# Kernel tuning notes

Measured on AMD Instinct MI355X. Metric: run time of the kernel, lower is better.

## Reference

```python
import jax, jax.numpy as jnp
import numpy as np

B, S, D, H, HD, F, V = 16, 512, 256, 8, 32, 682, 32000
EPS = 1.1920928955078125e-07


def rmsnorm(x, w):
    return x * jax.lax.rsqrt(jnp.mean(x * x, axis=-1, keepdims=True) + EPS) * w


def rope(x, cos, sin):
    # interleaved RoPE: even/odd lanes rotated pairwise, re-interleaved
    xe, xo = x[..., ::2], x[..., 1::2]
    return jnp.stack([xe * cos - xo * sin, xe * sin + xo * cos], axis=-1).reshape(x.shape)


def setup_inputs() -> dict:
    key = jax.random.key(0)
    ks = jax.random.split(key, 12)
    def n(k, shape, s=0.02):
        return jax.random.normal(k, shape, jnp.float32) * s
    pos = jnp.arange(S, dtype=jnp.float32)
    inv = 1.0 / (10000.0 ** (jnp.arange(0, HD, 2, dtype=jnp.float32) / HD))
    ang = pos[:, None] * inv[None, :]                      # [S, HD/2]
    cos_tab = jnp.repeat(jnp.cos(ang), 2, axis=-1)         # [S, HD]
    sin_tab = jnp.repeat(jnp.sin(ang), 2, axis=-1)
    mask = jnp.tril(jnp.ones((S, S), jnp.int32))[None, None]  # causal [1,1,S,S]
    return dict(
        emb=n(ks[0], (V, D)),
        pos_emb=n(ks[1], (S, D)),
        attn_norm_w=jnp.ones((D,), jnp.float32),
        wq=n(ks[2], (D, D)), bq=jnp.zeros((D,), jnp.float32),
        wk=n(ks[3], (HD, D)), bk=jnp.zeros((HD,), jnp.float32),
        wv=n(ks[4], (D, D)), bv=jnp.zeros((D,), jnp.float32),
        cos_tab=cos_tab, sin_tab=sin_tab,
        ffn_norm_w=jnp.ones((D,), jnp.float32),
        w_gate=n(ks[5], (F, D)), b_gate=jnp.zeros((F,), jnp.float32),
        w_up=n(ks[6], (F, D)), b_up=jnp.zeros((F,), jnp.float32),
        w_down=n(ks[7], (D, F)), b_down=jnp.zeros((D,), jnp.float32),
        tok_ids=jax.random.randint(ks[8], (B, S), 0, V, jnp.int64),
        mask=mask,
    )


def reference(emb, pos_emb, attn_norm_w, wq, bq, wk, bk, wv, bv, cos_tab, sin_tab,
              ffn_norm_w, w_gate, b_gate, w_up, b_up, w_down, b_down, tok_ids, mask):
    h = emb[tok_ids] + pos_emb                                   # [B,S,D]
    x = rmsnorm(h, attn_norm_w)
    # faithful to trace: direct view [B,S,D] -> [B,H,S,HD] (no transpose)
    q = (x @ wq.T + bq).reshape(B, H, S, HD)
    k = (x @ wk.T + bk)[:, None]                                 # [B,1,S,HD] single KV head
    v = (x @ wv.T + bv).reshape(B, H, S, HD)
    cos = cos_tab[:S, ::2][None, None]                           # [1,1,S,HD/2]
    sin = sin_tab[:S, ::2][None, None]
    qr = rope(q, cos, sin)
    kr = rope(k, cos, sin)[:, 0]                                 # [B,S,HD]
    scores = jnp.einsum('bhsd,btd->bhst', qr, kr) / jnp.sqrt(jnp.float32(HD))
    scores = jnp.where(mask == 0, -jnp.inf, scores)
    attn = jax.nn.softmax(scores, axis=-1)
    o = jnp.einsum('bhst,bhtd->bhsd', attn, v).reshape(B, S, D)
    h2 = o + h
    x2 = rmsnorm(h2, ffn_norm_w)
    g = x2 @ w_gate.T + b_gate
    g = g * jax.nn.sigmoid(g)                                    # SiLU gate
    up = x2 @ w_up.T + b_up
    out = (g * up) @ w_down.T + b_down
    # faithful to trace: residual uses post-norm activation x2, not h2
    return out + x2
```

## Files before the change

### kernel.cpp

```cpp
#include <hip/hip_runtime.h>
#include <hip/hip_bf16.h>
#include <cstddef>
#include <cstdint>

constexpr int Bb = 16, Ss = 512, Dd = 256, Hh = 8, HDd = 32, Ff = 682;
constexpr int FKp = 704;
constexpr float EPSf = 1.1920928955078125e-07f;

typedef short bf8v __attribute__((ext_vector_type(8)));
typedef float f4 __attribute__((ext_vector_type(4)));
using bf16 = __hip_bfloat16;

__device__ inline f4 MFMA(bf8v a, bf8v b, f4 c) {
  return __builtin_amdgcn_mfma_f32_16x16x32_bf16(a, b, c, 0, 0, 0);
}

__global__ __launch_bounds__(256) void k_prep(
    const float* __restrict__ wq, const float* __restrict__ wk,
    const float* __restrict__ wv, const float* __restrict__ wg,
    const float* __restrict__ wu, const float* __restrict__ wd,
    bf16* __restrict__ dqkv, bf16* __restrict__ dgate,
    bf16* __restrict__ dup, bf16* __restrict__ ddown,
    const float* __restrict__ emb, const float* __restrict__ pos,
    const int* __restrict__ tok, const float* __restrict__ w,
    bf16* __restrict__ hb, bf16* __restrict__ xb)
{
  const int b = blockIdx.x, tid = threadIdx.x;
  if (b < 640) {
    const int idx = b * 256 + tid;
    const int row = idx >> 8, col = idx & 255;
    float v;
    if (row < 256)      v = wq[(size_t)row * 256 + col];
    else if (row < 288) v = wk[(size_t)(row - 256) * 256 + col];
    else if (row < 544) v = wv[(size_t)(row - 288) * 256 + col];
    else                v = 0.f;
    dqkv[idx] = __float2bfloat16(v);
  } else if (b < 2176) {
    const bool isg = b < 1408;
    const int idx = (b - (isg ? 640 : 1408)) * 256 + tid;
    const int row = idx >> 8, col = idx & 255;
    const float* src = isg ? wg : wu;
    float v = (row < Ff) ? src[(size_t)row * 256 + col] : 0.f;
    (isg ? dgate : dup)[idx] = __float2bfloat16(v);
  } else if (b < 2880) {
    const int idx = (b - 2176) * 256 + tid;
    const int row = idx / FKp, col = idx - row * FKp;
    float v = (col < Ff) ? wd[(size_t)row * Ff + col] : 0.f;
    ddown[idx] = __float2bfloat16(v);
  } else {
    const int row = b - 2880;
    const int s = row & (Ss - 1);
    const int t = tok[row];
    float v = emb[(size_t)t * Dd + tid] + pos[(size_t)s * Dd + tid];
    float ss = v * v;
    #pragma unroll
    for (int off = 32; off > 0; off >>= 1) ss += __shfl_down(ss, off);
    __shared__ float red[4];
    if ((tid & 63) == 0) red[tid >> 6] = ss;
    __syncthreads();
    const float tot = red[0] + red[1] + red[2] + red[3];
    const float r = rsqrtf(tot * (1.0f / Dd) + EPSf);
    const size_t o = (size_t)row * Dd + tid;
    hb[o] = __float2bfloat16(v);
    xb[o] = __float2bfloat16(v * r * w[tid]);
  }
}

__global__ __launch_bounds__(256) void k_add_norm(
    const bf16* __restrict__ a, const bf16* __restrict__ hb,
    const float* __restrict__ w, bf16* __restrict__ x2b)
{
  const int row = blockIdx.x;
  const int tid = threadIdx.x;
  const size_t off = (size_t)row * Dd + tid;
  const float v = __bfloat162float(a[off]) + __bfloat162float(hb[off]);
  float ss = v * v;
  #pragma unroll
  for (int o = 32; o > 0; o >>= 1) ss += __shfl_down(ss, o);
  __shared__ float red[4];
  if ((tid & 63) == 0) red[tid >> 6] = ss;
  __syncthreads();
  const float tot = red[0] + red[1] + red[2] + red[3];
  const float r = rsqrtf(tot * (1.0f / Dd) + EPSf);
  x2b[off] = __float2bfloat16(v * r * w[tid]);
}

__global__ __launch_bounds__(256) void k_qkv(
    const bf16* __restrict__ A, const bf16* __restrict__ W,
    const float* __restrict__ bias0, const float* __restrict__ bias1,
    const float* __restrict__ bias2,
    const float* __restrict__ cost, const float* __restrict__ sint,
    bf16* __restrict__ ob0, bf16* __restrict__ ob1, bf16* __restrict__ vt)
{
  __shared__ bf16 As[128 * 72];
  __shared__ bf16 Bs[64 * 72];
  const int tid = threadIdx.x, lane = tid & 63, wid = tid >> 6;
  const int l15 = lane & 15, lg = lane >> 4;
  const int m0 = blockIdx.x * 128, n0 = blockIdx.y * 64;
  const int wr = (wid >> 1) * 64, wc = (wid & 1) * 32;
  const int srow = tid >> 3, scol = (tid & 7) * 8;

  f4 acc[4][2];
  #pragma unroll
  for (int i = 0; i < 4; i++)
    #pragma unroll
    for (int j = 0; j < 2; j++) acc[i][j] = (f4){0.f, 0.f, 0.f, 0.f};

  bf8v pa[4], pb[2];
  #pragma unroll
  for (int i = 0; i < 4; i++)
    pa[i] = *(const bf8v*)&A[(size_t)(m0 + srow + i * 32) * 256 + scol];
  #pragma unroll
  for (int i = 0; i < 2; i++)
    pb[i] = *(const bf8v*)&W[(size_t)(n0 + srow + i * 32) * 256 + scol];
  #pragma unroll
  for (int i = 0; i < 4; i++) *(bf8v*)&As[(srow + i * 32) * 72 + scol] = pa[i];
  #pragma unroll
  for (int i = 0; i < 2; i++) *(bf8v*)&Bs[(srow + i * 32) * 72 + scol] = pb[i];
  __syncthreads();

  for (int ks = 0; ks < 4; ks++) {
    if (ks < 3) {
      const int kn = (ks + 1) * 64;
      #pragma unroll
      for (int i = 0; i < 4; i++)
        pa[i] = *(const bf8v*)&A[(size_t)(m0 + srow + i * 32) * 256 + kn + scol];
      #pragma unroll
      for (int i = 0; i < 2; i++)
        pb[i] = *(const bf8v*)&W[(size_t)(n0 + srow + i * 32) * 256 + kn + scol];
    }
    #pragma unroll
    for (int kk = 0; kk < 64; kk += 32) {
      bf8v af[4], bw[2];
      #pragma unroll
      for (int mi = 0; mi < 4; mi++)
        af[mi] = *(const bf8v*)&As[(wr + mi * 16 + l15) * 72 + kk + lg * 8];
      #pragma unroll
      for (int ni = 0; ni < 2; ni++)
        bw[ni] = *(const bf8v*)&Bs[(wc + ni * 16 + l15) * 72 + kk + lg * 8];
      #pragma unroll
      for (int mi = 0; mi < 4; mi++)
        #pragma unroll
        for (int ni = 0; ni < 2; ni++)
          acc[mi][ni] = MFMA(af[mi], bw[ni], acc[mi][ni]);
    }
    __syncthreads();
    if (ks < 3) {
      #pragma unroll
      for (int i = 0; i < 4; i++) *(bf8v*)&As[(srow + i * 32) * 72 + scol] = pa[i];
      #pragma unroll
      for (int i = 0; i < 2; i++) *(bf8v*)&Bs[(srow + i * 32) * 72 + scol] = pb[i];
      __syncthreads();
    }
  }

  #pragma unroll
  for (int mi = 0; mi < 4; mi++) {
    #pragma unroll
    for (int ni = 0; ni < 2; ni++) {
      const int nbase = n0 + wc + ni * 16;
      const int n = nbase + l15;
      if (nbase < 288) {
        #pragma unroll
        for (int r = 0; r < 4; r++) {
          const int m = m0 + wr + mi * 16 + lg * 4 + r;
          float vb2 = acc[mi][ni][r] + (nbase < 256 ? bias0[n] : bias1[n - 256]);
          int s, hd;
          if (nbase < 256) { const int flat = ((m & 511) << 8) + n; s = (flat >> 5) & 511; hd = n & 31; }
          else             { s = m & 511; hd = n - 256; }
          const float c = cost[s * 32 + hd], sn = sint[s * 32 + hd];
          const float other = __shfl_xor(vb2, 1);
          const float res = (n & 1) ? (other * sn + vb2 * c) : (vb2 * c - other * sn);
          if (nbase < 256) ob0[(size_t)m * 256 + n] = __float2bfloat16(res);
          else             ob1[(size_t)m * 32 + hd] = __float2bfloat16(res);
        }
      } else if (nbase < 544) {
        const int rel = n - 288;
        const int hd = rel & 31, rq = rel >> 5;
        const int mb = m0 + wr + mi * 16 + lg * 4;
        const int b = mb >> 9;
        const float bv = bias2[rel];
        #pragma unroll
        for (int r = 0; r < 4; r++) {
          const int s = (mb + r) & 511;
          const int hh2 = s >> 6;
          const int s4 = ((s & 63) << 3) + rq;
          vt[((size_t)(b * Hh + hh2) * HDd + hd) * Ss + s4] =
              __float2bfloat16(acc[mi][ni][r] + bv);
        }
      }
    }
  }
}

__global__ __launch_bounds__(256) void k_ffn(
    const bf16* __restrict__ A, const bf16* __restrict__ Wg,
    const bf16* __restrict__ Wu,
    const float* __restrict__ bg, const float* __restrict__ bu,
    bf16* __restrict__ out)
{
  __shared__ bf16 As[128 * 72];
  __shared__ bf16 Gs[64 * 72];
  __shared__ bf16 Us[64 * 72];
  const int tid = threadIdx.x, lane = tid & 63, wid = tid >> 6;
  const int l15 = lane & 15, lg = lane >> 4;
  const int m0 = blockIdx.x * 128, n0 = blockIdx.y * 64;
  const int wr = (wid >> 1) * 64, wc = (wid & 1) * 32;
  const int srow = tid >> 3, scol = (tid & 7) * 8;

  f4 accg[4][2], accu[4][2];
  #pragma unroll
  for (int i = 0; i < 4; i++)
    #pragma unroll
    for (int j = 0; j < 2; j++) {
      accg[i][j] = (f4){0.f, 0.f, 0.f, 0.f};
      accu[i][j] = (f4){0.f, 0.f, 0.f, 0.f};
    }

  bf8v pa[4], pg[2], pu[2];
  #pragma unroll
  for (int i = 0; i < 4; i++)
    pa[i] = *(const bf8v*)&A[(size_t)(m0 + srow + i * 32) * 256 + scol];
  #pragma unroll
  for (int i = 0; i < 2; i++) {
    pg[i] = *(const bf8v*)&Wg[(size_t)(n0 + srow + i * 32) * 256 + scol];
    pu[i] = *(const bf8v*)&Wu[(size_t)(n0 + srow + i * 32) * 256 + scol];
  }
  #pragma unroll
  for (int i = 0; i < 4; i++) *(bf8v*)&As[(srow + i * 32) * 72 + scol] = pa[i];
  #pragma unroll
  for (int i = 0; i < 2; i++) {
    *(bf8v*)&Gs[(srow + i * 32) * 72 + scol] = pg[i];
    *(bf8v*)&Us[(srow + i * 32) * 72 + scol] = pu[i];
  }
  __syncthreads();

  for (int ks = 0; ks < 4; ks++) {
    if (ks < 3) {
      const int kn = (ks + 1) * 64;
      #pragma unroll
      for (int i = 0; i < 4; i++)
        pa[i] = *(const bf8v*)&A[(size_t)(m0 + srow + i * 32) * 256 + kn + scol];
      #pragma unroll
      for (int i = 0; i < 2; i++) {
        pg[i] = *(const bf8v*)&Wg[(size_t)(n0 + srow + i * 32) * 256 + kn + scol];
        pu[i] = *(const bf8v*)&Wu[(size_t)(n0 + srow + i * 32) * 256 + kn + scol];
      }
    }
    #pragma unroll
    for (int kk = 0; kk < 64; kk += 32) {
      bf8v af[4], bgf[2], buf[2];
      #pragma unroll
      for (int mi = 0; mi < 4; mi++)
        af[mi] = *(const bf8v*)&As[(wr + mi * 16 + l15) * 72 + kk + lg * 8];
      #pragma unroll
      for (int ni = 0; ni < 2; ni++) {
        bgf[ni] = *(const bf8v*)&Gs[(wc + ni * 16 + l15) * 72 + kk + lg * 8];
        buf[ni] = *(const bf8v*)&Us[(wc + ni * 16 + l15) * 72 + kk + lg * 8];
      }
      #pragma unroll
      for (int mi = 0; mi < 4; mi++)
        #pragma unroll
        for (int ni = 0; ni < 2; ni++) {
          accg[mi][ni] = MFMA(af[mi], bgf[ni], accg[mi][ni]);
          accu[mi][ni] = MFMA(af[mi], buf[ni], accu[mi][ni]);
        }
    }
    __syncthreads();
    if (ks < 3) {
      #pragma unroll
      for (int i = 0; i < 4; i++) *(bf8v*)&As[(srow + i * 32) * 72 + scol] = pa[i];
      #pragma unroll
      for (int i = 0; i < 2; i++) {
        *(bf8v*)&Gs[(srow + i * 32) * 72 + scol] = pg[i];
        *(bf8v*)&Us[(srow + i * 32) * 72 + scol] = pu[i];
      }
      __syncthreads();
    }
  }

  #pragma unroll
  for (int ni = 0; ni < 2; ni++) {
    const int n = n0 + wc + ni * 16 + l15;
    const float bgv = (n < Ff) ? bg[n] : 0.f;
    const float buv = (n < Ff) ? bu[n] : 0.f;
    #pragma unroll
    for (int mi = 0; mi < 4; mi++) {
      #pragma unroll
      for (int r = 0; r < 4; r++) {
        const int m = m0 + wr + mi * 16 + lg * 4 + r;
        float res = 0.f;
        if (n < Ff) {
          const float gv = accg[mi][ni][r] + bgv;
          const float uv = accu[mi][ni][r] + buv;
          res = gv / (1.f + __expf(-gv)) * uv;
        }
        out[(size_t)m * FKp + n] = __float2bfloat16(res);
      }
    }
  }
}

__global__ __launch_bounds__(256) void k_down(
    const bf16* __restrict__ A, const bf16* __restrict__ W,
    const float* __restrict__ bias, const bf16* __restrict__ resid,
    float* __restrict__ out)
{
  __shared__ bf16 As[64 * 72];
  __shared__ bf16 Bs[64 * 72];
  const int tid = threadIdx.x, lane = tid & 63, wid = tid >> 6;
  const int l15 = lane & 15, lg = lane >> 4;
  const int m0 = blockIdx.x * 64, n0 = blockIdx.y * 64;
  const int wr = (wid >> 1) * 32, wc = (wid & 1) * 32;
  const int srow = tid >> 3, scol = (tid & 7) * 8;

  f4 acc[2][2];
  #pragma unroll
  for (int i = 0; i < 2; i++)
    #pragma unroll
    for (int j = 0; j < 2; j++) acc[i][j] = (f4){0.f, 0.f, 0.f, 0.f};

  bf8v pa[2], pb[2];
  #pragma unroll
  for (int i = 0; i < 2; i++) {
    pa[i] = *(const bf8v*)&A[(size_t)(m0 + srow + i * 32) * FKp + scol];
    pb[i] = *(const bf8v*)&W[(size_t)(n0 + srow + i * 32) * FKp + scol];
  }
  #pragma unroll
  for (int i = 0; i < 2; i++) {
    *(bf8v*)&As[(srow + i * 32) * 72 + scol] = pa[i];
    *(bf8v*)&Bs[(srow + i * 32) * 72 + scol] = pb[i];
  }
  __syncthreads();

  for (int ks = 0; ks < 11; ks++) {
    if (ks < 10) {
      const int kn = (ks + 1) * 64;
      #pragma unroll
      for (int i = 0; i < 2; i++) {
        pa[i] = *(const bf8v*)&A[(size_t)(m0 + srow + i * 32) * FKp + kn + scol];
        pb[i] = *(const bf8v*)&W[(size_t)(n0 + srow + i * 32) * FKp + kn + scol];
      }
    }
    #pragma unroll
    for (int kk = 0; kk < 64; kk += 32) {
      bf8v af[2], bw[2];
      #pragma unroll
      for (int mi = 0; mi < 2; mi++)
        af[mi] = *(const bf8v*)&As[(wr + mi * 16 + l15) * 72 + kk + lg * 8];
      #pragma unroll
      for (int ni = 0; ni < 2; ni++)
        bw[ni] = *(const bf8v*)&Bs[(wc + ni * 16 + l15) * 72 + kk + lg * 8];
      #pragma unroll
      for (int mi = 0; mi < 2; mi++)
        #pragma unroll
        for (int ni = 0; ni < 2; ni++)
          acc[mi][ni] = MFMA(af[mi], bw[ni], acc[mi][ni]);
    }
    __syncthreads();
    if (ks < 10) {
      #pragma unroll
      for (int i = 0; i < 2; i++) {
        *(bf8v*)&As[(srow + i * 32) * 72 + scol] = pa[i];
        *(bf8v*)&Bs[(srow + i * 32) * 72 + scol] = pb[i];
      }
      __syncthreads();
    }
  }

  #pragma unroll
  for (int ni = 0; ni < 2; ni++) {
    const int n = n0 + wc + ni * 16 + l15;
    const float bv = bias[n];
    #pragma unroll
    for (int mi = 0; mi < 2; mi++) {
      #pragma unroll
      for (int r = 0; r < 4; r++) {
        const int m = m0 + wr + mi * 16 + lg * 4 + r;
        out[(size_t)m * 256 + n] = acc[mi][ni][r] + bv +
            __bfloat162float(resid[(size_t)m * 256 + n]);
      }
    }
  }
}

__global__ __launch_bounds__(64) void k_attn_mfma(
    const bf16* __restrict__ q, const bf16* __restrict__ k,
    const bf16* __restrict__ vt, bf16* __restrict__ o)
{
  __shared__ bf16 Ps[16 * 72];
  const int lane = threadIdx.x;
  const int l15 = lane & 15, lg = lane >> 4;
  const int hh = blockIdx.y, bb = blockIdx.z;
  const int bh = bb * Hh + hh;
  const int qrow = (31 - blockIdx.x) * 16;
  const int lt = (qrow + 15) >> 6;
  const float scale = 0.17677669529663687f;

  const bf16* kg = k + (size_t)bb * Ss * HDd;
  const bf16* vg = vt + (size_t)bh * (Ss * HDd);

  const bf8v qf = *(const bf8v*)&q[((size_t)bh * Ss + qrow + l15) * HDd + lg * 8];

  f4 oacc[2];
  oacc[0] = (f4){0.f, 0.f, 0.f, 0.f};
  oacc[1] = (f4){0.f, 0.f, 0.f, 0.f};
  float m = -3.0e38f, l = 0.f;

  for (int ti = 0; ti <= lt; ti++) {
    const int t0 = ti * 64;

    f4 sf[4];
    __builtin_amdgcn_s_setprio(1);
    #pragma unroll
    for (int tf = 0; tf < 4; tf++) {
      const bf8v kf = *(const bf8v*)&kg[(size_t)(t0 + tf * 16 + l15) * HDd + lg * 8];
      sf[tf] = MFMA(kf, qf, (f4){0.f, 0.f, 0.f, 0.f});
    }
    __builtin_amdgcn_s_setprio(0);

    bf8v vb[2][2];
    #pragma unroll
    for (int kt = 0; kt < 2; kt++)
      #pragma unroll
      for (int hf = 0; hf < 2; hf++)
        vb[kt][hf] = *(const bf8v*)&vg[(size_t)(hf * 16 + l15) * Ss + t0 + kt * 32 + lg * 8];

    float pm = -3.0e38f;
    if (ti == lt) {
      #pragma unroll
      for (int tf = 0; tf < 4; tf++)
        #pragma unroll
        for (int r = 0; r < 4; r++) {
          float sv = sf[tf][r] * scale;
          if (t0 + tf * 16 + lg * 4 + r > qrow + l15) sv = -3.0e38f;
          sf[tf][r] = sv;
          pm = fmaxf(pm, sv);
        }
    } else {
      #pragma unroll
      for (int tf = 0; tf < 4; tf++)
        #pragma unroll
        for (int r = 0; r < 4; r++) {
          const float sv = sf[tf][r] * scale;
          sf[tf][r] = sv;
          pm = fmaxf(pm, sv);
        }
    }
    pm = fmaxf(pm, __shfl_xor(pm, 16));
    pm = fmaxf(pm, __shfl_xor(pm, 32));

    const float nm = fmaxf(m, pm);
    const float corr = __expf(m - nm);
    m = nm;

    float ls = 0.f;
    #pragma unroll
    for (int tf = 0; tf < 4; tf++)
      #pragma unroll
      for (int r = 0; r < 4; r++) {
        const float p = __expf(sf[tf][r] - m);
        sf[tf][r] = p;
        ls += p;
      }
    ls += __shfl_xor(ls, 16);
    ls += __shfl_xor(ls, 32);
    l = l * corr + ls;

    #pragma unroll
    for (int tf = 0; tf < 4; tf++) {
      bf16 t4[4];
      #pragma unroll
      for (int r = 0; r < 4; r++) t4[r] = __float2bfloat16(sf[tf][r]);
      *(uint2*)&Ps[l15 * 72 + tf * 16 + lg * 4] = *(const uint2*)t4;
    }

    float corrT[4];
    #pragma unroll
    for (int r = 0; r < 4; r++) corrT[r] = __shfl(corr, lg * 4 + r);
    #pragma unroll
    for (int hf = 0; hf < 2; hf++)
      #pragma unroll
      for (int r = 0; r < 4; r++) oacc[hf][r] *= corrT[r];

    __builtin_amdgcn_s_setprio(1);
    #pragma unroll
    for (int kt = 0; kt < 2; kt++) {
      const bf8v pv = *(const bf8v*)&Ps[l15 * 72 + kt * 32 + lg * 8];
      #pragma unroll
      for (int hf = 0; hf < 2; hf++)
        oacc[hf] = MFMA(pv, vb[kt][hf], oacc[hf]);
    }
    __builtin_amdgcn_s_setprio(0);
  }

  float lT[4];
  #pragma unroll
  for (int r = 0; r < 4; r++) lT[r] = __shfl(l, lg * 4 + r);
  #pragma unroll
  for (int hf = 0; hf < 2; hf++)
    #pragma unroll
    for (int r = 0; r < 4; r++)
      o[((size_t)bh * Ss + qrow + lg * 4 + r) * HDd + hf * 16 + l15] =
          __float2bfloat16(oacc[hf][r] / lT[r]);
}

extern "C" void kernel_launch(void* const* d_in, const int* in_sizes, int n_in,
                              void* d_out, int out_size, void* d_ws, size_t ws_size,
                              hipStream_t stream)
{
  const float* emb     = (const float*)d_in[0];
  const float* pos_emb = (const float*)d_in[1];
  const float* attn_w  = (const float*)d_in[2];
  const float* wq      = (const float*)d_in[3];
  const float* bq      = (const float*)d_in[4];
  const float* wk      = (const float*)d_in[5];
  const float* bk      = (const float*)d_in[6];
  const float* wv      = (const float*)d_in[7];
  const float* bv      = (const float*)d_in[8];
  const float* cos_t   = (const float*)d_in[9];
  const float* sin_t   = (const float*)d_in[10];
  const float* ffn_w   = (const float*)d_in[11];
  const float* w_gate  = (const float*)d_in[12];
  const float* b_gate  = (const float*)d_in[13];
  const float* w_up    = (const float*)d_in[14];
  const float* b_up    = (const float*)d_in[15];
  const float* w_down  = (const float*)d_in[16];
  const float* b_down  = (const float*)d_in[17];
  const int*   tok     = (const int*)d_in[18];
  float* out = (float*)d_out;

  const size_t NT = (size_t)Bb * Ss;
  char* base = (char*)d_ws;
  size_t off = 0;
  auto alloc = [&](size_t bytes) {
    void* r = base + off;
    off = (off + bytes + 255) & ~(size_t)255;
    return r;
  };
  bf16*  h_bf   = (bf16*)alloc(NT * Dd * 2);
  bf16*  x_bf   = (bf16*)alloc(NT * Dd * 2);
  bf16*  q_bf   = (bf16*)alloc(NT * Dd * 2);
  bf16*  k_bf   = (bf16*)alloc(NT * HDd * 2);
  bf16*  vt_bf  = (bf16*)alloc(NT * Dd * 2);
  bf16*  o_bf   = (bf16*)alloc(NT * Dd * 2);
  bf16*  x2_bf  = (bf16*)alloc(NT * Dd * 2);
  bf16*  g_bf   = (bf16*)alloc(NT * (size_t)FKp * 2);
  bf16*  wqkv_b = (bf16*)alloc((size_t)640 * 256 * 2);
  bf16*  wgate_b= (bf16*)alloc((size_t)768 * 256 * 2);
  bf16*  wup_b  = (bf16*)alloc((size_t)768 * 256 * 2);
  bf16*  wdown_b= (bf16*)alloc((size_t)256 * FKp * 2);

  k_prep<<<dim3(2880 + NT), 256, 0, stream>>>(
      wq, wk, wv, w_gate, w_up, w_down, wqkv_b, wgate_b, wup_b, wdown_b,
      emb, pos_emb, tok, attn_w, h_bf, x_bf);

  k_qkv<<<dim3(NT / 128, 10), 256, 0, stream>>>(
      x_bf, wqkv_b, bq, bk, bv, cos_t, sin_t, q_bf, k_bf, vt_bf);

  k_attn_mfma<<<dim3(32, Hh, Bb), 64, 0, stream>>>(q_bf, k_bf, vt_bf, o_bf);

  k_add_norm<<<dim3(NT), 256, 0, stream>>>(o_bf, h_bf, ffn_w, x2_bf);

  k_ffn<<<dim3(NT / 128, 11), 256, 0, stream>>>(
      x2_bf, wgate_b, wup_b, b_gate, b_up, g_bf);

  k_down<<<dim3(NT / 64, 4), 256, 0, stream>>>(
      g_bf, wdown_b, b_down, x2_bf, out);
}
```

Measured before the change: 90.47 us.

## Stage GEMM tiles via direct global-to-LDS loads in qkv, ffn, down kernels

Replaces the register-staged, software-prefetched global->LDS copy in the three GEMM kernels with global_load_lds 16-byte direct loads into unpadded 64-wide LDS rows. This removes the VGPR round trip and LDS store instructions, which may lower register pressure. In exchange it drops the prefetch overlap: each k-step now loads and then waits at a barrier before computing. It also removes the 72-element padding, so the fragment reads may now hit LDS bank conflicts.

```diff
diff --git a/kernel.cpp b/kernel.cpp
--- a/kernel.cpp
+++ b/kernel.cpp
@@ -13,6 +13,12 @@
 
 __device__ inline f4 MFMA(bf8v a, bf8v b, f4 c) {
   return __builtin_amdgcn_mfma_f32_16x16x32_bf16(a, b, c, 0, 0, 0);
+}
+
+__device__ __forceinline__ void gl_lds16(const bf16* g, bf16* l) {
+  __builtin_amdgcn_global_load_lds(
+      (const __attribute__((address_space(1))) unsigned int*)(g),
+      (__attribute__((address_space(3))) unsigned int*)(l), 16, 0, 0);
 }
 
 __global__ __launch_bounds__(256) void k_prep(
@@ -92,13 +98,13 @@
     const float* __restrict__ cost, const float* __restrict__ sint,
     bf16* __restrict__ ob0, bf16* __restrict__ ob1, bf16* __restrict__ vt)
 {
-  __shared__ bf16 As[128 * 72];
-  __shared__ bf16 Bs[64 * 72];
-  const int tid = threadIdx.x, lane = tid & 63, wid = tid >> 6;
+  __shared__ bf16 As[128 * 64];
+  __shared__ bf16 Bs[64 * 64];
+  const int tid = threadIdx.x, lane = tid & 63, wv = tid >> 6;
   const int l15 = lane & 15, lg = lane >> 4;
   const int m0 = blockIdx.x * 128, n0 = blockIdx.y * 64;
-  const int wr = (wid >> 1) * 64, wc = (wid & 1) * 32;
-  const int srow = tid >> 3, scol = (tid & 7) * 8;
+  const int wr = (wv >> 1) * 64, wc = (wv & 1) * 32;
+  const int sr8 = lane >> 3, slot = lane & 7;
 
   f4 acc[4][2];
   #pragma unroll
@@ -106,52 +112,37 @@
     #pragma unroll
     for (int j = 0; j < 2; j++) acc[i][j] = (f4){0.f, 0.f, 0.f, 0.f};
 
-  bf8v pa[4], pb[2];
-  #pragma unroll
-  for (int i = 0; i < 4; i++)
-    pa[i] = *(const bf8v*)&A[(size_t)(m0 + srow + i * 32) * 256 + scol];
-  #pragma unroll
-  for (int i = 0; i < 2; i++)
-    pb[i] = *(const bf8v*)&W[(size_t)(n0 + srow + i * 32) * 256 + scol];
-  #pragma unroll
-  for (int i = 0; i < 4; i++) *(bf8v*)&As[(srow + i * 32) * 72 + scol] = pa[i];
-  #pragma unroll
-  for (int i = 0; i < 2; i++) *(bf8v*)&Bs[(srow + i * 32) * 72 + scol] = pb[i];
-  __syncthreads();
-
   for (int ks = 0; ks < 4; ks++) {
-    if (ks < 3) {
-      const int kn = (ks + 1) * 64;
-      #pragma unroll
-      for (int i = 0; i < 4; i++)
-        pa[i] = *(const bf8v*)&A[(size_t)(m0 + srow + i * 32) * 256 + kn + scol];
-      #pragma unroll
-      for (int i = 0; i < 2; i++)
-        pb[i] = *(const bf8v*)&W[(size_t)(n0 + srow + i * 32) * 256 + kn + scol];
-    }
+    const int k0 = ks * 64;
+    #pragma unroll
+    for (int i = 0; i < 4; i++) {
+      const int row = wv * 32 + i * 8 + sr8;
+      gl_lds16(&A[(size_t)(m0 + row) * 256 + k0 + slot * 8],
+               &As[(wv * 32 + i * 8) * 64]);
+    }
+    #pragma unroll
+    for (int i = 0; i < 2; i++) {
+      const int row = wv * 16 + i * 8 + sr8;
+      gl_lds16(&W[(size_t)(n0 + row) * 256 + k0 + slot * 8],
+               &Bs[(wv * 16 + i * 8) * 64]);
+    }
+    __syncthreads();
     #pragma unroll
     for (int kk = 0; kk < 64; kk += 32) {
       bf8v af[4], bw[2];
       #pragma unroll
       for (int mi = 0; mi < 4; mi++)
-        af[mi] = *(const bf8v*)&As[(wr + mi * 16 + l15) * 72 + kk + lg * 8];
+        af[mi] = *(const bf8v*)&As[(wr + mi * 16 + l15) * 64 + kk + lg * 8];
       #pragma unroll
       for (int ni = 0; ni < 2; ni++)
-        bw[ni] = *(const bf8v*)&Bs[(wc + ni * 16 + l15) * 72 + kk + lg * 8];
+        bw[ni] = *(const bf8v*)&Bs[(wc + ni * 16 + l15) * 64 + kk + lg * 8];
       #pragma unroll
       for (int mi = 0; mi < 4; mi++)
         #pragma unroll
         for (int ni = 0; ni < 2; ni++)
           acc[mi][ni] = MFMA(af[mi], bw[ni], acc[mi][ni]);
     }
-    __syncthreads();
-    if (ks < 3) {
-      #pragma unroll
-      for (int i = 0; i < 4; i++) *(bf8v*)&As[(srow + i * 32) * 72 + scol] = pa[i];
-      #pragma unroll
-      for (int i = 0; i < 2; i++) *(bf8v*)&Bs[(srow + i * 32) * 72 + scol] = pb[i];
-      __syncthreads();
-    }
+    if (ks < 3) __syncthreads();
   }
 
   #pragma unroll
@@ -199,14 +190,14 @@
     const float* __restrict__ bg, const float* __restrict__ bu,
     bf16* __restrict__ out)
 {
-  __shared__ bf16 As[128 * 72];
-  __shared__ bf16 Gs[64 * 72];
-  __shared__ bf16 Us[64 * 72];
-  const int tid = threadIdx.x, lane = tid & 63, wid = tid >> 6;
+  __shared__ bf16 As[128 * 64];
+  __shared__ bf16 Gs[64 * 64];
+  __shared__ bf16 Us[64 * 64];
+  const int tid = threadIdx.x, lane = tid & 63, wv = tid >> 6;
   const int l15 = lane & 15, lg = lane >> 4;
   const int m0 = blockIdx.x * 128, n0 = blockIdx.y * 64;
-  const int wr = (wid >> 1) * 64, wc = (wid & 1) * 32;
-  const int srow = tid >> 3, scol = (tid & 7) * 8;
+  const int wr = (wv >> 1) * 64, wc = (wv & 1) * 32;
+  const int sr8 = lane >> 3, slot = lane & 7;
 
   f4 accg[4][2], accu[4][2];
   #pragma unroll
@@ -217,46 +208,33 @@
       accu[i][j] = (f4){0.f, 0.f, 0.f, 0.f};
     }
 
-  bf8v pa[4], pg[2], pu[2];
-  #pragma unroll
-  for (int i = 0; i < 4; i++)
-    pa[i] = *(const bf8v*)&A[(size_t)(m0 + srow + i * 32) * 256 + scol];
-  #pragma unroll
-  for (int i = 0; i < 2; i++) {
-    pg[i] = *(const bf8v*)&Wg[(size_t)(n0 + srow + i * 32) * 256 + scol];
-    pu[i] = *(const bf8v*)&Wu[(size_t)(n0 + srow + i * 32) * 256 + scol];
-  }
-  #pragma unroll
-  for (int i = 0; i < 4; i++) *(bf8v*)&As[(srow + i * 32) * 72 + scol] = pa[i];
-  #pragma unroll
-  for (int i = 0; i < 2; i++) {
-    *(bf8v*)&Gs[(srow + i * 32) * 72 + scol] = pg[i];
-    *(bf8v*)&Us[(srow + i * 32) * 72 + scol] = pu[i];
-  }
-  __syncthreads();
-
   for (int ks = 0; ks < 4; ks++) {
-    if (ks < 3) {
-      const int kn = (ks + 1) * 64;
-      #pragma unroll
-      for (int i = 0; i < 4; i++)
-        pa[i] = *(const bf8v*)&A[(size_t)(m0 + srow + i * 32) * 256 + kn + scol];
-      #pragma unroll
-      for (int i = 0; i < 2; i++) {
-        pg[i] = *(const bf8v*)&Wg[(size_t)(n0 + srow + i * 32) * 256 + kn + scol];
-        pu[i] = *(const bf8v*)&Wu[(size_t)(n0 + srow + i * 32) * 256 + kn + scol];
-      }
-    }
+    const int k0 = ks * 64;
+    #pragma unroll
+    for (int i = 0; i < 4; i++) {
+      const int row = wv * 32 + i * 8 + sr8;
+      gl_lds16(&A[(size_t)(m0 + row) * 256 + k0 + slot * 8],
+               &As[(wv * 32 + i * 8) * 64]);
+    }
+    #pragma unroll
+    for (int i = 0; i < 2; i++) {
+      const int row = wv * 16 + i * 8 + sr8;
+      gl_lds16(&Wg[(size_t)(n0 + row) * 256 + k0 + slot * 8],
+               &Gs[(wv * 16 + i * 8) * 64]);
+      gl_lds16(&Wu[(size_t)(n0 + row) * 256 + k0 + slot * 8],
+               &Us[(wv * 16 + i * 8) * 64]);
+    }
+    __syncthreads();
     #pragma unroll
     for (int kk = 0; kk < 64; kk += 32) {
       bf8v af[4], bgf[2], buf[2];
       #pragma unroll
       for (int mi = 0; mi < 4; mi++)
-        af[mi] = *(const bf8v*)&As[(wr + mi * 16 + l15) * 72 + kk + lg * 8];
+        af[mi] = *(const bf8v*)&As[(wr + mi * 16 + l15) * 64 + kk + lg * 8];
       #pragma unroll
       for (int ni = 0; ni < 2; ni++) {
-        bgf[ni] = *(const bf8v*)&Gs[(wc + ni * 16 + l15) * 72 + kk + lg * 8];
-        buf[ni] = *(const bf8v*)&Us[(wc + ni * 16 + l15) * 72 + kk + lg * 8];
+        bgf[ni] = *(const bf8v*)&Gs[(wc + ni * 16 + l15) * 64 + kk + lg * 8];
+        buf[ni] = *(const bf8v*)&Us[(wc + ni * 16 + l15) * 64 + kk + lg * 8];
       }
       #pragma unroll
       for (int mi = 0; mi < 4; mi++)
@@ -266,17 +244,7 @@
           accu[mi][ni] = MFMA(af[mi], buf[ni], accu[mi][ni]);
         }
     }
-    __syncthreads();
-    if (ks < 3) {
-      #pragma unroll
-      for (int i = 0; i < 4; i++) *(bf8v*)&As[(srow + i * 32) * 72 + scol] = pa[i];
-      #pragma unroll
-      for (int i = 0; i < 2; i++) {
-        *(bf8v*)&Gs[(srow + i * 32) * 72 + scol] = pg[i];
-        *(bf8v*)&Us[(srow + i * 32) * 72 + scol] = pu[i];
-      }
-      __syncthreads();
-    }
+    if (ks < 3) __syncthreads();
   }
 
   #pragma unroll
@@ -306,13 +274,13 @@
     const float* __restrict__ bias, const bf16* __restrict__ resid,
     float* __restrict__ out)
 {
-  __shared__ bf16 As[64 * 72];
-  __shared__ bf16 Bs[64 * 72];
-  const int tid = threadIdx.x, lane = tid & 63, wid = tid >> 6;
+  __shared__ bf16 As[64 * 64];
+  __shared__ bf16 Bs[64 * 64];
+  const int tid = threadIdx.x, lane = tid & 63, wv = tid >> 6;
   const int l15 = lane & 15, lg = lane >> 4;
   const int m0 = blockIdx.x * 64, n0 = blockIdx.y * 64;
-  const int wr = (wid >> 1) * 32, wc = (wid & 1) * 32;
-  const int srow = tid >> 3, scol = (tid & 7) * 8;
+  const int wr = (wv >> 1) * 32, wc = (wv & 1) * 32;
+  const int sr8 = lane >> 3, slot = lane & 7;
 
   f4 acc[2][2];
   #pragma unroll
@@ -320,52 +288,33 @@
     #pragma unroll
     for (int j = 0; j < 2; j++) acc[i][j] = (f4){0.f, 0.f, 0.f, 0.f};
 
-  bf8v pa[2], pb[2];
-  #pragma unroll
-  for (int i = 0; i < 2; i++) {
-    pa[i] = *(const bf8v*)&A[(size_t)(m0 + srow + i * 32) * FKp + scol];
-    pb[i] = *(const bf8v*)&W[(size_t)(n0 + srow + i * 32) * FKp + scol];
-  }
-  #pragma unroll
-  for (int i = 0; i < 2; i++) {
-    *(bf8v*)&As[(srow + i * 32) * 72 + scol] = pa[i];
-    *(bf8v*)&Bs[(srow + i * 32) * 72 + scol] = pb[i];
-  }
-  __syncthreads();
-
   for (int ks = 0; ks < 11; ks++) {
-    if (ks < 10) {
-      const int kn = (ks + 1) * 64;
-      #pragma unroll
-      for (int i = 0; i < 2; i++) {
-        pa[i] = *(const bf8v*)&A[(size_t)(m0 + srow + i * 32) * FKp + kn + scol];
-        pb[i] = *(const bf8v*)&W[(size_t)(n0 + srow + i * 32) * FKp + kn + scol];
-      }
-    }
+    const int k0 = ks * 64;
+    #pragma unroll
+    for (int i = 0; i < 2; i++) {
+      const int rowa = wv * 16 + i * 8 + sr8;
+      gl_lds16(&A[(size_t)(m0 + rowa) * FKp + k0 + slot * 8],
+               &As[(wv * 16 + i * 8) * 64]);
+      gl_lds16(&W[(size_t)(n0 + rowa) * FKp + k0 + slot * 8],
+               &Bs[(wv * 16 + i * 8) * 64]);
+    }
+    __syncthreads();
     #pragma unroll
     for (int kk = 0; kk < 64; kk += 32) {
       bf8v af[2], bw[2];
       #pragma unroll
       for (int mi = 0; mi < 2; mi++)
-        af[mi] = *(const bf8v*)&As[(wr + mi * 16 + l15) * 72 + kk + lg * 8];
+        af[mi] = *(const bf8v*)&As[(wr + mi * 16 + l15) * 64 + kk + lg * 8];
       #pragma unroll
       for (int ni = 0; ni < 2; ni++)
-        bw[ni] = *(const bf8v*)&Bs[(wc + ni * 16 + l15) * 72 + kk + lg * 8];
+        bw[ni] = *(const bf8v*)&Bs[(wc + ni * 16 + l15) * 64 + kk + lg * 8];
       #pragma unroll
       for (int mi = 0; mi < 2; mi++)
         #pragma unroll
         for (int ni = 0; ni < 2; ni++)
           acc[mi][ni] = MFMA(af[mi], bw[ni], acc[mi][ni]);
     }
-    __syncthreads();
-    if (ks < 10) {
-      #pragma unroll
-      for (int i = 0; i < 2; i++) {
-        *(bf8v*)&As[(srow + i * 32) * 72 + scol] = pa[i];
-        *(bf8v*)&Bs[(srow + i * 32) * 72 + scol] = pb[i];
-      }
-      __syncthreads();
-    }
+    if (ks < 10) __syncthreads();
   }
 
   #pragma unroll
```

New measurement: 90.74 us. About the same (+0.3%).

## Fuse residual add and FFN RMSNorm into attention epilogue with 8-head blocks

Applied to the files above, without the earlier changes.

The attention kernel now runs all 8 heads of a batch as 8 waves in one 512-thread block. Each wave adds the residual h and computes the RMSNorm directly on its output. This works because the raw [B,H,S,HD] to [B,S,D] view makes each group of 8 consecutive (row, head-dim) lanes form one normalized row. The change removes the separate add-norm kernel, one launch, and the round trip of the attention output through global memory. In exchange there are fewer, larger blocks with per-wave shared buffers, and the norm reduction relies on the view-layout mapping being exact.

```diff
diff --git a/kernel.cpp b/kernel.cpp
--- a/kernel.cpp
+++ b/kernel.cpp
@@ -66,25 +66,6 @@
   }
 }
 
-__global__ __launch_bounds__(256) void k_add_norm(
-    const bf16* __restrict__ a, const bf16* __restrict__ hb,
-    const float* __restrict__ w, bf16* __restrict__ x2b)
-{
-  const int row = blockIdx.x;
-  const int tid = threadIdx.x;
-  const size_t off = (size_t)row * Dd + tid;
-  const float v = __bfloat162float(a[off]) + __bfloat162float(hb[off]);
-  float ss = v * v;
-  #pragma unroll
-  for (int o = 32; o > 0; o >>= 1) ss += __shfl_down(ss, o);
-  __shared__ float red[4];
-  if ((tid & 63) == 0) red[tid >> 6] = ss;
-  __syncthreads();
-  const float tot = red[0] + red[1] + red[2] + red[3];
-  const float r = rsqrtf(tot * (1.0f / Dd) + EPSf);
-  x2b[off] = __float2bfloat16(v * r * w[tid]);
-}
-
 __global__ __launch_bounds__(256) void k_qkv(
     const bf16* __restrict__ A, const bf16* __restrict__ W,
     const float* __restrict__ bias0, const float* __restrict__ bias1,
@@ -384,15 +365,16 @@
   }
 }
 
-__global__ __launch_bounds__(64) void k_attn_mfma(
+__global__ __launch_bounds__(512) void k_attn_norm(
     const bf16* __restrict__ q, const bf16* __restrict__ k,
-    const bf16* __restrict__ vt, bf16* __restrict__ o)
+    const bf16* __restrict__ vt, const bf16* __restrict__ hb,
+    const float* __restrict__ w, bf16* __restrict__ x2b)
 {
-  __shared__ bf16 Ps[16 * 72];
-  const int lane = threadIdx.x;
+  __shared__ bf16 Ps[8][16 * 72];
+  const int tid = threadIdx.x, lane = tid & 63, wid = tid >> 6;
   const int l15 = lane & 15, lg = lane >> 4;
-  const int hh = blockIdx.y, bb = blockIdx.z;
-  const int bh = bb * Hh + hh;
+  const int bb = blockIdx.y;
+  const int bh = bb * Hh + wid;
   const int qrow = (31 - blockIdx.x) * 16;
   const int lt = (qrow + 15) >> 6;
   const float scale = 0.17677669529663687f;
@@ -472,7 +454,7 @@
       bf16 t4[4];
       #pragma unroll
       for (int r = 0; r < 4; r++) t4[r] = __float2bfloat16(sf[tf][r]);
-      *(uint2*)&Ps[l15 * 72 + tf * 16 + lg * 4] = *(const uint2*)t4;
+      *(uint2*)&Ps[wid][l15 * 72 + tf * 16 + lg * 4] = *(const uint2*)t4;
     }
 
     float corrT[4];
@@ -486,7 +468,7 @@
     __builtin_amdgcn_s_setprio(1);
     #pragma unroll
     for (int kt = 0; kt < 2; kt++) {
-      const bf8v pv = *(const bf8v*)&Ps[l15 * 72 + kt * 32 + lg * 8];
+      const bf8v pv = *(const bf8v*)&Ps[wid][l15 * 72 + kt * 32 + lg * 8];
       #pragma unroll
       for (int hf = 0; hf < 2; hf++)
         oacc[hf] = MFMA(pv, vb[kt][hf], oacc[hf]);
@@ -497,12 +479,38 @@
   float lT[4];
   #pragma unroll
   for (int r = 0; r < 4; r++) lT[r] = __shfl(l, lg * 4 + r);
+
+  const size_t bbase = (size_t)bb * (Ss * Dd);
+  float vv[2][4];
   #pragma unroll
   for (int hf = 0; hf < 2; hf++)
     #pragma unroll
-    for (int r = 0; r < 4; r++)
-      o[((size_t)bh * Ss + qrow + lg * 4 + r) * HDd + hf * 16 + l15] =
-          __float2bfloat16(oacc[hf][r] / lT[r]);
+    for (int r = 0; r < 4; r++) {
+      const int frow = qrow + lg * 4 + r;
+      const int hd = hf * 16 + l15;
+      vv[hf][r] = oacc[hf][r] / lT[r] +
+          __bfloat162float(hb[bbase + (size_t)wid * 16384 + frow * 32 + hd]);
+    }
+
+  float ss = 0.f;
+  #pragma unroll
+  for (int hf = 0; hf < 2; hf++)
+    #pragma unroll
+    for (int r = 0; r < 4; r++) ss += vv[hf][r] * vv[hf][r];
+  #pragma unroll
+  for (int x = 1; x < 32; x <<= 1) ss += __shfl_xor(ss, x);
+  const float rr = rsqrtf(ss * (1.0f / Dd) + EPSf);
+
+  #pragma unroll
+  for (int hf = 0; hf < 2; hf++)
+    #pragma unroll
+    for (int r = 0; r < 4; r++) {
+      const int frow = qrow + lg * 4 + r;
+      const int hd = hf * 16 + l15;
+      const int d2 = ((frow & 7) << 5) + hd;
+      x2b[bbase + (size_t)wid * 16384 + frow * 32 + hd] =
+          __float2bfloat16(vv[hf][r] * rr * w[d2]);
+    }
 }
 
 extern "C" void kernel_launch(void* const* d_in, const int* in_sizes, int n_in,
@@ -543,7 +551,6 @@
   bf16*  q_bf   = (bf16*)alloc(NT * Dd * 2);
   bf16*  k_bf   = (bf16*)alloc(NT * HDd * 2);
   bf16*  vt_bf  = (bf16*)alloc(NT * Dd * 2);
-  bf16*  o_bf   = (bf16*)alloc(NT * Dd * 2);
   bf16*  x2_bf  = (bf16*)alloc(NT * Dd * 2);
   bf16*  g_bf   = (bf16*)alloc(NT * (size_t)FKp * 2);
   bf16*  wqkv_b = (bf16*)alloc((size_t)640 * 256 * 2);
@@ -558,9 +565,8 @@
   k_qkv<<<dim3(NT / 128, 10), 256, 0, stream>>>(
       x_bf, wqkv_b, bq, bk, bv, cos_t, sin_t, q_bf, k_bf, vt_bf);
 
-  k_attn_mfma<<<dim3(32, Hh, Bb), 64, 0, stream>>>(q_bf, k_bf, vt_bf, o_bf);
-
-  k_add_norm<<<dim3(NT), 256, 0, stream>>>(o_bf, h_bf, ffn_w, x2_bf);
+  k_attn_norm<<<dim3(32, Bb), 512, 0, stream>>>(
+      q_bf, k_bf, vt_bf, h_bf, ffn_w, x2_bf);
 
   k_ffn<<<dim3(NT / 128, 11), 256, 0, stream>>>(
       x2_bf, wgate_b, wup_b, b_gate, b_up, g_bf);
```

After: 84.16 us. 7.0% less time.
